# Kernel tuning notes

Hardware: AMD Instinct MI355X
Metric: run time of the kernel (lower is better)

The kernel has to match this reference:

```python
import jax, jax.numpy as jnp
import numpy as np

DIM, K, G, PAD = 384, 3, 4, 1
KK = K * K
EPS = 1e-5


def _deform_conv(x, offset, weight):
    # x: [B,C,H,W]; offset: [B,G*2*KK,H,W] (per group: (dy,dx) per tap); weight: [Cout,Cin,K,K]
    B, C, H, W = x.shape
    Cg = C // G
    off = offset.reshape(B, G, KK, 2, H, W)
    dy, dx = off[:, :, :, 0], off[:, :, :, 1]            # [B,G,KK,H,W]
    ky = (jnp.arange(KK) // K - PAD).astype(x.dtype).reshape(1, 1, KK, 1, 1)
    kx = (jnp.arange(KK) % K - PAD).astype(x.dtype).reshape(1, 1, KK, 1, 1)
    py = dy + ky + jnp.arange(H, dtype=x.dtype).reshape(1, 1, 1, H, 1)
    px = dx + kx + jnp.arange(W, dtype=x.dtype).reshape(1, 1, 1, 1, W)

    y0 = jnp.floor(py); x0 = jnp.floor(px)
    iy0 = y0.astype(jnp.int32); ix0 = x0.astype(jnp.int32)
    wy1 = py - y0; wx1 = px - x0
    img = x.reshape(B, G, Cg, H * W)[:, :, :, None, :]   # [B,G,Cg,1,HW]

    def corner(iy, ix, w):
        valid = (iy >= 0) & (iy < H) & (ix >= 0) & (ix < W)
        idx = (jnp.clip(iy, 0, H - 1) * W + jnp.clip(ix, 0, W - 1)).reshape(B, G, 1, KK, H * W)
        vals = jnp.take_along_axis(img, idx, axis=-1)    # [B,G,Cg,KK,HW]
        wm = (w * valid.astype(x.dtype)).reshape(B, G, 1, KK, H * W)
        return vals * wm

    sampled = (corner(iy0, ix0, (1 - wy1) * (1 - wx1))
               + corner(iy0, ix0 + 1, (1 - wy1) * wx1)
               + corner(iy0 + 1, ix0, wy1 * (1 - wx1))
               + corner(iy0 + 1, ix0 + 1, wy1 * wx1))    # [B,G,Cg,KK,HW]
    sampled = sampled.reshape(B, C, KK, H * W)
    out = jnp.einsum('bckp,ock->bop', sampled, weight.reshape(C, C, KK))
    return out.reshape(B, C, H, W)


def setup_inputs() -> dict:
    key = jax.random.key(0)
    ks = jax.random.split(key, 8)
    B, H, W = 8, 32, 32
    off_ch = G * 2 * KK
    return {
        'x': jax.random.normal(ks[0], (B, H * W, DIM), jnp.float32),
        'w_off': jax.random.normal(ks[1], (off_ch, DIM, 3, 3), jnp.float32) * 0.01,
        'b_off': jnp.zeros((off_ch,), jnp.float32),
        'w_dcn': jax.random.normal(ks[2], (DIM, DIM, K, K), jnp.float32) * 0.02,
        'bn_gamma': jnp.ones((DIM,), jnp.float32) + 0.1 * jax.random.normal(ks[3], (DIM,), jnp.float32),
        'bn_beta': 0.1 * jax.random.normal(ks[4], (DIM,), jnp.float32),
        'bn_mean': 0.1 * jax.random.normal(ks[5], (DIM,), jnp.float32),
        'bn_var': jax.random.uniform(ks[6], (DIM,), jnp.float32, 0.5, 1.5),
        'w2': jax.random.normal(ks[7], (DIM, DIM), jnp.float32) * 0.05,
        'b2': jnp.zeros((DIM,), jnp.float32),
        'H': H, 'W': W,
    }


def reference(x, w_off, b_off, w_dcn, bn_gamma, bn_beta, bn_mean, bn_var, w2, b2, H, W):
    B, P, C = x.shape
    xi = x.transpose(0, 2, 1).reshape(B, C, H, W)                       # [B,C,H,W]
    offset = jax.lax.conv_general_dilated(xi, w_off, (1, 1), ((1, 1), (1, 1)),
                                          dimension_numbers=('NCHW', 'OIHW', 'NCHW'))
    offset = offset + b_off[None, :, None, None]
    y = _deform_conv(xi, offset, w_dcn)
    # eval-mode BatchNorm2d + SiLU
    scale = bn_gamma / jnp.sqrt(bn_var + EPS)
    y = y * scale[None, :, None, None] + (bn_beta - bn_mean * scale)[None, :, None, None]
    y = y * jax.nn.sigmoid(y)
    # 1x1 conv
    y = jnp.einsum('bchw,oc->bohw', y, w2) + b2[None, :, None, None]
    return y.reshape(B, C, H * W).transpose(0, 2, 1)
```

## Files before the change

kernel.cpp:

```cpp
#include <hip/hip_runtime.h>
#include <math.h>

typedef _Float16 f16;
typedef _Float16 f16x2 __attribute__((ext_vector_type(2)));
typedef _Float16 f16x4 __attribute__((ext_vector_type(4)));
typedef _Float16 f16x8 __attribute__((ext_vector_type(8)));
typedef float f32x4 __attribute__((ext_vector_type(4)));

#define EPS_ 1e-5f

#define N_XP   3551232
#define N_WDCN 1327104
#define N_WOFF 331776
#define N_W2   147456
#define N_OFFS 589824
#define N_YH   3145728
#define N_AS   28311552

#define WS_NEED ((size_t)(N_XP + N_WDCN + N_WOFF + N_W2 + N_AS + N_YH) * 2 + (size_t)N_OFFS * 4)

static __device__ __forceinline__ f16x8 sp8(f16 h) { return (f16x8){h,h,h,h,h,h,h,h}; }

#define GLD_LDS16(g, l) __builtin_amdgcn_global_load_lds( \
    (const __attribute__((address_space(1))) void*)(g),   \
    (__attribute__((address_space(3))) void*)(l), 16, 0, 0)

#define VMCNT(N) asm volatile("s_waitcnt vmcnt(" #N ")" ::: "memory")

#define PK_X   786432
#define PK_XP  101376
#define PK_WD  147456
#define PK_WO  27648
#define PK_WZ  10368
#define PK_W2  147456
__global__ void k_pack(const float* __restrict__ x, const float* __restrict__ w_off,
                       const float* __restrict__ w_dcn, const float* __restrict__ w2,
                       f16* __restrict__ xp, f16* __restrict__ woffp,
                       f16* __restrict__ wdcnp, f16* __restrict__ w2p) {
    long i = (long)blockIdx.x * 256 + threadIdx.x;
    if (i < PK_X) {
        float4 v = ((const float4*)x)[i];
        f16x4 hv; hv.x = (f16)v.x; hv.y = (f16)v.y; hv.z = (f16)v.z; hv.w = (f16)v.w;
        int m = (int)(i / 96), c4 = (int)(i % 96);
        int b = m >> 10, h = (m >> 5) & 31, w = m & 31;
        long idx = ((long)(b * 34 + h + 1) * 34 + (w + 1)) * 96 + c4;
        ((f16x4*)xp)[idx] = hv;
    } else if (i < PK_X + PK_XP) {
        int j = (int)(i - PK_X);
        int cell = j / 96, c4 = j % 96;
        int b = cell / 132, p = cell % 132;
        int r, cp;
        if (p < 34)       { r = 0;          cp = p; }
        else if (p < 68)  { r = 33;         cp = p - 34; }
        else if (p < 100) { r = p - 68 + 1; cp = 0; }
        else              { r = p - 100 + 1; cp = 33; }
        long idx = ((long)(b * 34 + r) * 34 + cp) * 96 + c4;
        ((f16x4*)xp)[idx] = (f16x4){};
    } else if (i < PK_X + PK_XP + PK_WD) {
        int j = (int)(i - PK_X - PK_XP);
        int c = j % 384, oc = j / 384;
#pragma unroll
        for (int kk = 0; kk < 9; ++kk) {
            f16 v = (f16)w_dcn[(long)j * 9 + kk];
            wdcnp[(long)(kk * 6 + (c >> 6)) * 24576 + oc * 64 + (c & 63)] = v;
        }
    } else if (i < PK_X + PK_XP + PK_WD + PK_WO) {
        int j = (int)(i - PK_X - PK_XP - PK_WD);
        int c = j % 384, oc = j / 384;
#pragma unroll
        for (int kk = 0; kk < 9; ++kk) {
            f16 v = (f16)w_off[(long)j * 9 + kk];
            woffp[(long)(kk * 6 + (c >> 6)) * 6144 + oc * 64 + (c & 63)] = v;
        }
    } else if (i < PK_X + PK_XP + PK_WD + PK_WO + PK_WZ) {
        int j = (int)(i - PK_X - PK_XP - PK_WD - PK_WO);
        int ck = j / 192, r = j % 192;
        *(f16x8*)(&woffp[(long)ck * 6144 + 72 * 64 + r * 8]) = (f16x8){};
    } else if (i < PK_X + PK_XP + PK_WD + PK_WO + PK_WZ + PK_W2) {
        long j = i - (PK_X + PK_XP + PK_WD + PK_WO + PK_WZ);
        int kc = (int)(j & 63); long r = j >> 6;
        int oc = (int)(r % 384); int cc = (int)(r / 384);
        w2p[j] = (f16)w2[(long)oc * 384 + cc * 64 + kc];
    }
}

__global__ __launch_bounds__(256, 2) void k_off_gemm4(
        const f16* __restrict__ xp, const f16* __restrict__ wp,
        float* __restrict__ part) {
    __shared__ __attribute__((aligned(16))) f16 As[4][64 * 64];
    __shared__ __attribute__((aligned(16))) f16 Bs[4][96 * 64];
    int t = threadIdx.x;
    int bx = blockIdx.x;
    int ks = blockIdx.y;
    bx = (bx & 7) * 16 + (bx >> 3);
    int m0 = bx * 64;
    int w = t >> 6, l = t & 63, lr = l & 15, lq = l >> 4;
    int wmi = w & 1, wni = w >> 1;
    f32x4 acc[2][3] = {};

    const f16* a_base[2];
#pragma unroll
    for (int i = 0; i < 2; ++i) {
        int f = i * 256 + t;
        int ml = f >> 3, c8 = f & 7;
        int m = m0 + ml;
        int b = m >> 10, h = (m >> 5) & 31, ww = m & 31;
        a_base[i] = xp + ((long)(b * 34 + h + 1) * 34 + (ww + 1)) * 384 + ((c8 ^ (ml & 7)) * 8);
    }
    const f16* b_src[3];
#pragma unroll
    for (int i = 0; i < 3; ++i) {
        int f = i * 256 + t;
        int oc = f >> 3, c8 = f & 7;
        b_src[i] = wp + (long)oc * 64 + ((c8 ^ (oc & 7)) * 8);
    }

    int s_ck = (54 * ks) >> 2, e_ck = (54 * (ks + 1)) >> 2;
    int nck = e_ck - s_ck;

    auto stage = [&](int j, int buf) {
        int ck = s_ck + j;
        int kk = ck / 6, cc = ck % 6;
        int kkd = ((kk / 3 - 1) * 34 + (kk % 3 - 1)) * 384 + cc * 64;
#pragma unroll
        for (int i = 0; i < 2; ++i)
            GLD_LDS16(a_base[i] + kkd, &As[buf][i * 2048 + w * 512]);
#pragma unroll
        for (int i = 0; i < 3; ++i)
            GLD_LDS16(b_src[i] + (long)ck * 6144, &Bs[buf][i * 2048 + w * 512]);
    };
    auto compute = [&](int buf) {
        const char* Ab = (const char*)&As[buf][0];
        const char* Bb = (const char*)&Bs[buf][0];
        __builtin_amdgcn_s_setprio(1);
#pragma unroll
        for (int s = 0; s < 2; ++s) {
            int j = (s << 2) | lq;
            int swz = (j ^ (lr & 7)) * 16;
            f16x8 af[2], bf[3];
#pragma unroll
            for (int mi = 0; mi < 2; ++mi)
                af[mi] = *(const f16x8*)(Ab + (wmi * 32 + mi * 16 + lr) * 128 + swz);
#pragma unroll
            for (int n = 0; n < 3; ++n)
                bf[n] = *(const f16x8*)(Bb + (wni * 48 + n * 16 + lr) * 128 + swz);
#pragma unroll
            for (int mi = 0; mi < 2; ++mi)
#pragma unroll
                for (int n = 0; n < 3; ++n)
                    acc[mi][n] = __builtin_amdgcn_mfma_f32_16x16x32_f16(af[mi], bf[n], acc[mi][n], 0, 0, 0);
        }
        __builtin_amdgcn_s_setprio(0);
    };

    stage(0, 0);
    stage(1, 1);
    for (int j = 0; j < nck; ++j) {
        if (j + 2 < nck) {
            stage(j + 2, (j + 2) & 3);
            VMCNT(10);
        } else if (j + 1 < nck) {
            VMCNT(5);
        } else {
            VMCNT(0);
        }
        __builtin_amdgcn_s_barrier();
        compute(j & 3);
    }
    float* pb = part + (long)ks * (96 * 8192);
#pragma unroll
    for (int n = 0; n < 3; ++n) {
        int oc = wni * 48 + 16 * n + lr;
#pragma unroll
        for (int mi = 0; mi < 2; ++mi) {
            int m = m0 + wmi * 32 + 16 * mi + 4 * lq;
            *(f32x4*)(&pb[(long)oc * 8192 + m]) = acc[mi][n];
        }
    }
}

__global__ __launch_bounds__(256) void k_off_reduce(
        const float* __restrict__ part, const float* __restrict__ b_off,
        float* __restrict__ offs) {
    int j = blockIdx.x * 256 + threadIdx.x;
    int oc = j >> 11;
    int mq = (j & 2047) << 2;
    const long S = 96L * 8192;
    f32x4 s0 = *(const f32x4*)(&part[(long)oc * 8192 + mq]);
    f32x4 s1 = *(const f32x4*)(&part[S + (long)oc * 8192 + mq]);
    f32x4 s2 = *(const f32x4*)(&part[2 * S + (long)oc * 8192 + mq]);
    f32x4 s3 = *(const f32x4*)(&part[3 * S + (long)oc * 8192 + mq]);
    f32x4 s = s0 + s1 + s2 + s3;
    float b = b_off[oc];
#pragma unroll
    for (int r = 0; r < 4; ++r)
        offs[(long)(mq + r) * 72 + oc] = s[r] + b;
}

__global__ __launch_bounds__(256) void k_sample(
        const f16* __restrict__ xp, const float* __restrict__ offs,
        f16* __restrict__ A_t) {
    __shared__ int   cad[64][4][4];
    __shared__ f16x4 cwd[64][4];
    int t = threadIdx.x;
    int raw = blockIdx.x;
    int bx = (raw & 7) * 16 + (raw >> 3);
    int kk = blockIdx.y;
    int m0 = bx * 64;
    {
        int row = t & 63, g = t >> 6;
        int m = m0 + row;
        int b = m >> 10, h = (m >> 5) & 31, wpix = m & 31;
        const float2 o = *(const float2*)(offs + (long)m * 72 + (g * 9 + kk) * 2);
        float py = o.x + (float)(h + kk / 3 - 1);
        float px = o.y + (float)(wpix + kk % 3 - 1);
        float fy = floorf(py), fx = floorf(px);
        int iy0 = (int)fy, ix0 = (int)fx;
        float wy1 = py - fy, wx1 = px - fx;
        float wy0 = 1.f - wy1, wx0 = 1.f - wx1;
        bool vy0 = iy0 >= 0 && iy0 < 32, vy1 = iy0 + 1 >= 0 && iy0 + 1 < 32;
        bool vx0 = ix0 >= 0 && ix0 < 32, vx1 = ix0 + 1 >= 0 && ix0 + 1 < 32;
        int cy0 = min(max(iy0, 0), 31), cy1 = min(max(iy0 + 1, 0), 31);
        int cx0 = min(max(ix0, 0), 31), cx1 = min(max(ix0 + 1, 0), 31);
        cad[row][g][0] = ((b * 34 + cy0 + 1) * 34 + cx0 + 1) * 768;
        cad[row][g][1] = ((b * 34 + cy0 + 1) * 34 + cx1 + 1) * 768;
        cad[row][g][2] = ((b * 34 + cy1 + 1) * 34 + cx0 + 1) * 768;
        cad[row][g][3] = ((b * 34 + cy1 + 1) * 34 + cx1 + 1) * 768;
        f16x4 wv;
        wv.x = (f16)(wy0 * wx0 * ((vy0 && vx0) ? 1.f : 0.f));
        wv.y = (f16)(wy0 * wx1 * ((vy0 && vx1) ? 1.f : 0.f));
        wv.z = (f16)(wy1 * wx0 * ((vy1 && vx0) ? 1.f : 0.f));
        wv.w = (f16)(wy1 * wx1 * ((vy1 && vx1) ? 1.f : 0.f));
        cwd[row][g] = wv;
    }
    __syncthreads();
    int rb = t >> 3, w8 = t & 7;
    const char* xb = (const char*)xp;
    long obase = ((long)bx * 54 + (long)kk * 6) * 4096;
#pragma unroll
    for (int cc = 0; cc < 6; ++cc) {
        int c = cc * 64 + 8 * w8;
        int g = c / 96;
        long cb = (long)c * 2;
#pragma unroll
        for (int rr = 0; rr < 2; ++rr) {
            int r = 2 * rb + rr;
            const int* ca = cad[r][g];
            f16x4 wv = cwd[r][g];
            f16x8 v0 = *(const f16x8*)(xb + ca[0] + cb);
            f16x8 v1 = *(const f16x8*)(xb + ca[1] + cb);
            f16x8 v2 = *(const f16x8*)(xb + ca[2] + cb);
            f16x8 v3 = *(const f16x8*)(xb + ca[3] + cb);
            f16x8 ov = v0 * sp8(wv.x) + v1 * sp8(wv.y) + v2 * sp8(wv.z) + v3 * sp8(wv.w);
            *(f16x8*)(A_t + obase + cc * 4096 + r * 64 + ((w8 ^ (r & 7)) * 8)) = ov;
        }
    }
}

__global__ __launch_bounds__(256, 2) void k_dcn_gemm2(
        const f16* __restrict__ A_t, const f16* __restrict__ Bp,
        const float* __restrict__ bng, const float* __restrict__ bnb,
        const float* __restrict__ bnm, const float* __restrict__ bnv,
        f16* __restrict__ yh) {
    __shared__ __attribute__((aligned(16))) f16 As[4][64 * 64];
    __shared__ __attribute__((aligned(16))) f16 Bs[4][96 * 64];
    int t = threadIdx.x;
    int bx = blockIdx.x;
    bx = (bx & 7) * 16 + (bx >> 3);
    int m0 = bx * 64;
    int n0 = blockIdx.y * 96;
    int w = t >> 6, l = t & 63, lr = l & 15, lq = l >> 4;
    int wmi = w & 1, wni = w >> 1;
    f32x4 acc[2][3] = {};

    const f16* a_base = A_t + (long)bx * 54 * 4096 + t * 8;
    const f16* b_src[3];
#pragma unroll
    for (int i = 0; i < 3; ++i) {
        int f = i * 256 + t;
        int oc = f >> 3, c8 = f & 7;
        b_src[i] = Bp + (long)(n0 + oc) * 64 + ((c8 ^ (oc & 7)) * 8);
    }

    auto stage = [&](int ck, int buf) {
#pragma unroll
        for (int i = 0; i < 2; ++i)
            GLD_LDS16(a_base + (long)ck * 4096 + i * 2048, &As[buf][i * 2048 + w * 512]);
#pragma unroll
        for (int i = 0; i < 3; ++i)
            GLD_LDS16(b_src[i] + (long)ck * 24576, &Bs[buf][i * 2048 + w * 512]);
    };
    auto compute = [&](int buf) {
        const char* Ab = (const char*)&As[buf][0];
        const char* Bb = (const char*)&Bs[buf][0];
        __builtin_amdgcn_s_setprio(1);
#pragma unroll
        for (int s = 0; s < 2; ++s) {
            int j = (s << 2) | lq;
            int swz = (j ^ (lr & 7)) * 16;
            f16x8 af[2], bf[3];
#pragma unroll
            for (int mi = 0; mi < 2; ++mi)
                af[mi] = *(const f16x8*)(Ab + (wmi * 32 + mi * 16 + lr) * 128 + swz);
#pragma unroll
            for (int n = 0; n < 3; ++n)
                bf[n] = *(const f16x8*)(Bb + (wni * 48 + n * 16 + lr) * 128 + swz);
#pragma unroll
            for (int mi = 0; mi < 2; ++mi)
#pragma unroll
                for (int n = 0; n < 3; ++n)
                    acc[mi][n] = __builtin_amdgcn_mfma_f32_16x16x32_f16(af[mi], bf[n], acc[mi][n], 0, 0, 0);
        }
        __builtin_amdgcn_s_setprio(0);
    };

    stage(0, 0);
    stage(1, 1);
    for (int ck = 0; ck < 54; ++ck) {
        if (ck + 2 < 54) {
            stage(ck + 2, (ck + 2) & 3);
            VMCNT(10);
        } else if (ck + 1 < 54) {
            VMCNT(5);
        } else {
            VMCNT(0);
        }
        __builtin_amdgcn_s_barrier();
        compute(ck & 3);
    }
#pragma unroll
    for (int n = 0; n < 3; ++n) {
        int oc = n0 + wni * 48 + n * 16 + lr;
        float sc = bng[oc] * rsqrtf(bnv[oc] + EPS_);
        float shf = bnb[oc] - bnm[oc] * sc;
#pragma unroll
        for (int mi = 0; mi < 2; ++mi)
#pragma unroll
            for (int r = 0; r < 4; ++r) {
                int m = m0 + wmi * 32 + mi * 16 + 4 * lq + r;
                float v = acc[mi][n][r] * sc + shf;
                v = v / (1.f + __expf(-v));
                yh[(long)m * 384 + oc] = (f16)v;
            }
    }
}

__global__ __launch_bounds__(512, 2) void k_dcn_fused(
        const f16* __restrict__ xp, const float* __restrict__ offs,
        const f16* __restrict__ wp,
        const float* __restrict__ bng, const float* __restrict__ bnb,
        const float* __restrict__ bnm, const float* __restrict__ bnv,
        f16* __restrict__ yh) {
    __shared__ __attribute__((aligned(16))) f16 As[2][64 * 72];
    __shared__ __attribute__((aligned(16))) int ca[2][4][64][4];
    __shared__ __attribute__((aligned(16))) f16x4 cwl[2][4][64];
    int t = threadIdx.x;
    int bx = blockIdx.x;
    bx = (bx & 7) * 16 + (bx >> 3);
    int m0 = bx * 64;
    int n0 = blockIdx.y * 192;
    int w = t >> 6, l = t & 63, lr = l & 15, lq = l >> 4;
    int wm = (w & 1) * 32, wn = (w >> 1) * 48;
    int spx = t >> 3, slot = t & 7;
    const char* xb = (const char*)xp;
    f32x4 acc[2][3] = {};

    auto coords = [&](int kkn, int bufn) {
        if (t < 256) {
            int g = t >> 6, px = t & 63;
            int m = m0 + px;
            int b = m >> 10, h = (m >> 5) & 31, wwp = m & 31;
            int ky = kkn / 3 - 1, kx = kkn % 3 - 1;
            const float2 o = *(const float2*)(offs + (long)m * 72 + (g * 9 + kkn) * 2);
            float py = o.x + (float)(h + ky);
            float pxx = o.y + (float)(wwp + kx);
            float fy = floorf(py), fx = floorf(pxx);
            int iy0 = (int)fy, ix0 = (int)fx;
            float wy1 = py - fy, wx1 = pxx - fx;
            float wy0 = 1.f - wy1, wx0 = 1.f - wx1;
            bool vy0 = iy0 >= 0 && iy0 < 32, vy1 = iy0 + 1 >= 0 && iy0 + 1 < 32;
            bool vx0 = ix0 >= 0 && ix0 < 32, vx1 = ix0 + 1 >= 0 && ix0 + 1 < 32;
            int cy0 = min(max(iy0, 0), 31), cy1 = min(max(iy0 + 1, 0), 31);
            int cx0 = min(max(ix0, 0), 31), cx1 = min(max(ix0 + 1, 0), 31);
            ca[bufn][g][px][0] = ((b * 34 + cy0 + 1) * 34 + cx0 + 1) * 768;
            ca[bufn][g][px][1] = ((b * 34 + cy0 + 1) * 34 + cx1 + 1) * 768;
            ca[bufn][g][px][2] = ((b * 34 + cy1 + 1) * 34 + cx0 + 1) * 768;
            ca[bufn][g][px][3] = ((b * 34 + cy1 + 1) * 34 + cx1 + 1) * 768;
            f16x4 wv;
            wv.x = (f16)(wy0 * wx0 * ((vy0 && vx0) ? 1.f : 0.f));
            wv.y = (f16)(wy0 * wx1 * ((vy0 && vx1) ? 1.f : 0.f));
            wv.z = (f16)(wy1 * wx0 * ((vy1 && vx0) ? 1.f : 0.f));
            wv.w = (f16)(wy1 * wx1 * ((vy1 && vx1) ? 1.f : 0.f));
            cwl[bufn][g][px] = wv;
        }
    };

    coords(0, 0);
    __syncthreads();
    {
        int cst = 8 * slot;
        int g = cst / 96;
        int4 cv = *(const int4*)(&ca[0][g][spx][0]);
        f16x4 wv = cwl[0][g][spx];
        long cb = (long)(cst * 2);
        f16x8 v0 = *(const f16x8*)(xb + cv.x + cb);
        f16x8 v1 = *(const f16x8*)(xb + cv.y + cb);
        f16x8 v2 = *(const f16x8*)(xb + cv.z + cb);
        f16x8 v3 = *(const f16x8*)(xb + cv.w + cb);
        f16x8 sv = v0 * sp8(wv.x) + v1 * sp8(wv.y) + v2 * sp8(wv.z) + v3 * sp8(wv.w);
        *(f16x8*)(&As[0][spx * 72 + 8 * slot]) = sv;
    }
    int cur = 0, kk = 0, cc = 0;
    for (int ck = 0; ck < 54; ++ck) {
        __syncthreads();
        bool hn = ck < 53;
        int kk2 = kk + (cc == 5), cc2 = (cc == 5) ? 0 : (cc + 1);
        f16x8 v0, v1, v2, v3; f16x4 wv;
        if (hn) {
            int cst = cc2 * 64 + 8 * slot;
            int g = cst / 96;
            int kb = kk2 & 1;
            int4 cv = *(const int4*)(&ca[kb][g][spx][0]);
            wv = cwl[kb][g][spx];
            long cb = (long)(cst * 2);
            v0 = *(const f16x8*)(xb + cv.x + cb);
            v1 = *(const f16x8*)(xb + cv.y + cb);
            v2 = *(const f16x8*)(xb + cv.z + cb);
            v3 = *(const f16x8*)(xb + cv.w + cb);
        }
        if (cc == 4 && kk < 8) coords(kk + 1, (kk + 1) & 1);
        const f16* wbase = wp + (long)ck * (384 * 64);
#pragma unroll
        for (int s = 0; s < 2; ++s) {
            f16x8 a0 = *(const f16x8*)(&As[cur][(wm + lr) * 72 + 32 * s + 8 * lq]);
            f16x8 a1 = *(const f16x8*)(&As[cur][(wm + 16 + lr) * 72 + 32 * s + 8 * lq]);
#pragma unroll
            for (int n = 0; n < 3; ++n) {
                f16x8 b = *(const f16x8*)(wbase + (long)(n0 + wn + 16 * n + lr) * 64 + 32 * s + 8 * lq);
                acc[0][n] = __builtin_amdgcn_mfma_f32_16x16x32_f16(a0, b, acc[0][n], 0, 0, 0);
                acc[1][n] = __builtin_amdgcn_mfma_f32_16x16x32_f16(a1, b, acc[1][n], 0, 0, 0);
            }
        }
        if (hn) {
            f16x8 sv = v0 * sp8(wv.x) + v1 * sp8(wv.y) + v2 * sp8(wv.z) + v3 * sp8(wv.w);
            *(f16x8*)(&As[cur ^ 1][spx * 72 + 8 * slot]) = sv;
        }
        cur ^= 1; kk = kk2; cc = cc2;
    }
#pragma unroll
    for (int n = 0; n < 3; ++n) {
        int oc = n0 + wn + 16 * n + lr;
        float sc = bng[oc] * rsqrtf(bnv[oc] + EPS_);
        float sh = bnb[oc] - bnm[oc] * sc;
#pragma unroll
        for (int mi = 0; mi < 2; ++mi)
#pragma unroll
            for (int r = 0; r < 4; ++r) {
                int m = m0 + wm + 16 * mi + 4 * lq + r;
                float v = acc[mi][n][r] * sc + sh;
                v = v / (1.f + __expf(-v));
                yh[(long)m * 384 + oc] = (f16)v;
            }
    }
}

__global__ __launch_bounds__(256, 2) void k_out_gemm3(
        const f16* __restrict__ yh, const f16* __restrict__ wp,
        const float* __restrict__ b2, float* __restrict__ out) {
    __shared__ __attribute__((aligned(16))) f16 As[4][64 * 64];
    __shared__ __attribute__((aligned(16))) f16 Bs[4][96 * 64];
    int t = threadIdx.x;
    int bx = blockIdx.x;
    bx = (bx & 7) * 16 + (bx >> 3);
    int m0 = bx * 64;
    int n0 = blockIdx.y * 96;
    int w = t >> 6, l = t & 63, lr = l & 15, lq = l >> 4;
    int wmi = w & 1, wni = w >> 1;
    f32x4 acc[2][3] = {};

    const f16* a_src[2];
#pragma unroll
    for (int i = 0; i < 2; ++i) {
        int f = i * 256 + t;
        int ml = f >> 3, c8 = f & 7;
        a_src[i] = yh + (long)(m0 + ml) * 384 + ((c8 ^ (ml & 7)) * 8);
    }
    const f16* b_src[3];
#pragma unroll
    for (int i = 0; i < 3; ++i) {
        int f = i * 256 + t;
        int oc = f >> 3, c8 = f & 7;
        b_src[i] = wp + (long)(n0 + oc) * 64 + ((c8 ^ (oc & 7)) * 8);
    }

    auto stage = [&](int cc, int buf) {
#pragma unroll
        for (int i = 0; i < 2; ++i)
            GLD_LDS16(a_src[i] + cc * 64, &As[buf][i * 2048 + w * 512]);
#pragma unroll
        for (int i = 0; i < 3; ++i)
            GLD_LDS16(b_src[i] + (long)cc * 24576, &Bs[buf][i * 2048 + w * 512]);
    };
    auto compute = [&](int buf) {
        const char* Ab = (const char*)&As[buf][0];
        const char* Bb = (const char*)&Bs[buf][0];
        __builtin_amdgcn_s_setprio(1);
#pragma unroll
        for (int s = 0; s < 2; ++s) {
            int j = (s << 2) | lq;
            int swz = (j ^ (lr & 7)) * 16;
            f16x8 af[2], bf[3];
#pragma unroll
            for (int mi = 0; mi < 2; ++mi)
                af[mi] = *(const f16x8*)(Ab + (wmi * 32 + mi * 16 + lr) * 128 + swz);
#pragma unroll
            for (int n = 0; n < 3; ++n)
                bf[n] = *(const f16x8*)(Bb + (wni * 48 + n * 16 + lr) * 128 + swz);
#pragma unroll
            for (int mi = 0; mi < 2; ++mi)
#pragma unroll
                for (int n = 0; n < 3; ++n)
                    acc[mi][n] = __builtin_amdgcn_mfma_f32_16x16x32_f16(af[mi], bf[n], acc[mi][n], 0, 0, 0);
        }
        __builtin_amdgcn_s_setprio(0);
    };

    stage(0, 0);
    stage(1, 1);
    for (int cc = 0; cc < 6; ++cc) {
        if (cc + 2 < 6) {
            stage(cc + 2, (cc + 2) & 3);
            VMCNT(10);
        } else if (cc + 1 < 6) {
            VMCNT(5);
        } else {
            VMCNT(0);
        }
        __builtin_amdgcn_s_barrier();
        compute(cc & 3);
    }
#pragma unroll
    for (int n = 0; n < 3; ++n) {
        int oc = n0 + wni * 48 + 16 * n + lr;
        float bia = b2[oc];
#pragma unroll
        for (int mi = 0; mi < 2; ++mi)
#pragma unroll
            for (int r = 0; r < 4; ++r) {
                int m = m0 + wmi * 32 + 16 * mi + 4 * lq + r;
                out[(long)m * 384 + oc] = acc[mi][n][r] + bia;
            }
    }
}

extern "C" void kernel_launch(void* const* d_in, const int* in_sizes, int n_in,
                              void* d_out, int out_size, void* d_ws, size_t ws_size,
                              hipStream_t stream) {
    const float* x        = (const float*)d_in[0];
    const float* w_off    = (const float*)d_in[1];
    const float* b_off    = (const float*)d_in[2];
    const float* w_dcn    = (const float*)d_in[3];
    const float* bn_gamma = (const float*)d_in[4];
    const float* bn_beta  = (const float*)d_in[5];
    const float* bn_mean  = (const float*)d_in[6];
    const float* bn_var   = (const float*)d_in[7];
    const float* w2       = (const float*)d_in[8];
    const float* b2       = (const float*)d_in[9];

    char* ws = (char*)d_ws;
    f16*   xp    = (f16*)ws;                                  ws += (size_t)N_XP * 2;
    f16*   wdcnp = (f16*)ws;                                  ws += (size_t)N_WDCN * 2;
    f16*   woffp = (f16*)ws;                                  ws += (size_t)N_WOFF * 2;
    f16*   w2p   = (f16*)ws;                                  ws += (size_t)N_W2 * 2;
    float* offs  = (float*)ws;                                ws += (size_t)N_OFFS * 4;
    f16*   yh    = (f16*)ws;                                  ws += (size_t)N_YH * 2;
    f16*   A_t   = (f16*)ws;
    bool big = ws_size >= WS_NEED;
    float* part = (float*)(big ? (void*)A_t : (void*)ws);

    k_pack<<<4770, 256, 0, stream>>>(x, w_off, w_dcn, w2, xp, woffp, wdcnp, w2p);
    k_off_gemm4<<<dim3(128, 4), 256, 0, stream>>>(xp, woffp, part);
    k_off_reduce<<<576, 256, 0, stream>>>(part, b_off, offs);

    if (big) {
        k_sample<<<dim3(128, 9), 256, 0, stream>>>(xp, offs, A_t);
        k_dcn_gemm2<<<dim3(128, 4), 256, 0, stream>>>(A_t, wdcnp,
                bn_gamma, bn_beta, bn_mean, bn_var, yh);
    } else {
        k_dcn_fused<<<dim3(128, 2), 512, 0, stream>>>(xp, offs, wdcnp,
                bn_gamma, bn_beta, bn_mean, bn_var, yh);
    }
    k_out_gemm3<<<dim3(128, 4), 256, 0, stream>>>(yh, w2p, b2, (float*)d_out);
}
```

Baseline: 84.09 us.

## Load GEMM B fragments directly into registers and drop B shared-memory staging

In the deformable-conv GEMM and the output 1x1 GEMM, the weight (B) operand is now read from global memory straight into MFMA fragment registers, double-buffered across two k-chunks. It is no longer staged through swizzled LDS buffers. Removing the Bs arrays cuts LDS per block, so launch bounds are raised to allow 3 blocks per CU. The cost is duplicated global/L2 traffic for B across waves, more vector registers, and a retuned vmcnt wait scheme that has to match the new load counts.

Result: slower. 136.6 us (+62.4%).

```diff
diff --git a/kernel.cpp b/kernel.cpp
--- a/kernel.cpp
+++ b/kernel.cpp
@@ -257,13 +257,12 @@
     }
 }
 
-__global__ __launch_bounds__(256, 2) void k_dcn_gemm2(
+__global__ __launch_bounds__(256, 3) void k_dcn_gemm2(
         const f16* __restrict__ A_t, const f16* __restrict__ Bp,
         const float* __restrict__ bng, const float* __restrict__ bnb,
         const float* __restrict__ bnm, const float* __restrict__ bnv,
         f16* __restrict__ yh) {
     __shared__ __attribute__((aligned(16))) f16 As[4][64 * 64];
-    __shared__ __attribute__((aligned(16))) f16 Bs[4][96 * 64];
     int t = threadIdx.x;
     int bx = blockIdx.x;
     bx = (bx & 7) * 16 + (bx >> 3);
@@ -274,59 +273,57 @@
     f32x4 acc[2][3] = {};
 
     const f16* a_base = A_t + (long)bx * 54 * 4096 + t * 8;
-    const f16* b_src[3];
-#pragma unroll
-    for (int i = 0; i < 3; ++i) {
-        int f = i * 256 + t;
-        int oc = f >> 3, c8 = f & 7;
-        b_src[i] = Bp + (long)(n0 + oc) * 64 + ((c8 ^ (oc & 7)) * 8);
-    }
-
-    auto stage = [&](int ck, int buf) {
+    const f16* b_frag = Bp + (long)(n0 + wni * 48 + lr) * 64 + 8 * lq;
+
+    auto stageA = [&](int ck, int buf) {
 #pragma unroll
         for (int i = 0; i < 2; ++i)
             GLD_LDS16(a_base + (long)ck * 4096 + i * 2048, &As[buf][i * 2048 + w * 512]);
-#pragma unroll
-        for (int i = 0; i < 3; ++i)
-            GLD_LDS16(b_src[i] + (long)ck * 24576, &Bs[buf][i * 2048 + w * 512]);
-    };
-    auto compute = [&](int buf) {
+    };
+    auto ldB = [&](f16x8 bf[3][2], int ck) {
+        const f16* wb = b_frag + (long)ck * 24576;
+#pragma unroll
+        for (int n = 0; n < 3; ++n)
+#pragma unroll
+            for (int s = 0; s < 2; ++s)
+                bf[n][s] = *(const f16x8*)(wb + n * 16 * 64 + 32 * s);
+    };
+    auto compute = [&](int buf, f16x8 bf[3][2]) {
         const char* Ab = (const char*)&As[buf][0];
-        const char* Bb = (const char*)&Bs[buf][0];
         __builtin_amdgcn_s_setprio(1);
 #pragma unroll
         for (int s = 0; s < 2; ++s) {
             int j = (s << 2) | lq;
             int swz = (j ^ (lr & 7)) * 16;
-            f16x8 af[2], bf[3];
+            f16x8 af[2];
 #pragma unroll
             for (int mi = 0; mi < 2; ++mi)
                 af[mi] = *(const f16x8*)(Ab + (wmi * 32 + mi * 16 + lr) * 128 + swz);
 #pragma unroll
-            for (int n = 0; n < 3; ++n)
-                bf[n] = *(const f16x8*)(Bb + (wni * 48 + n * 16 + lr) * 128 + swz);
-#pragma unroll
             for (int mi = 0; mi < 2; ++mi)
 #pragma unroll
                 for (int n = 0; n < 3; ++n)
-                    acc[mi][n] = __builtin_amdgcn_mfma_f32_16x16x32_f16(af[mi], bf[n], acc[mi][n], 0, 0, 0);
+                    acc[mi][n] = __builtin_amdgcn_mfma_f32_16x16x32_f16(af[mi], bf[n][s], acc[mi][n], 0, 0, 0);
         }
         __builtin_amdgcn_s_setprio(0);
     };
 
-    stage(0, 0);
-    stage(1, 1);
-    for (int ck = 0; ck < 54; ++ck) {
-        if (ck + 2 < 54) {
-            stage(ck + 2, (ck + 2) & 3);
-            VMCNT(10);
-        } else if (ck + 1 < 54) {
-            VMCNT(5);
-        } else {
-            VMCNT(0);
-        }
+    f16x8 b0[3][2], b1[3][2];
+    stageA(0, 0);
+    stageA(1, 1);
+    ldB(b0, 0);
+    for (int c2 = 0; c2 < 27; ++c2) {
+        int ck = 2 * c2;
+        if (ck + 2 < 54) stageA(ck + 2, (ck + 2) & 3);
+        ldB(b1, ck + 1);
+        VMCNT(8);
         __builtin_amdgcn_s_barrier();
-        compute(ck & 3);
+        compute(ck & 3, b0);
+        if (ck + 3 < 54) stageA(ck + 3, (ck + 3) & 3);
+        if (ck + 2 < 54) { ldB(b0, ck + 2); VMCNT(8); }
+        else             { VMCNT(0); }
+        __builtin_amdgcn_s_barrier();
+        compute((ck + 1) & 3, b1);
     }
 #pragma unroll
     for (int n = 0; n < 3; ++n) {
@@ -464,11 +461,10 @@
     }
 }
 
-__global__ __launch_bounds__(256, 2) void k_out_gemm3(
+__global__ __launch_bounds__(256, 3) void k_out_gemm3(
         const f16* __restrict__ yh, const f16* __restrict__ wp,
         const float* __restrict__ b2, float* __restrict__ out) {
     __shared__ __attribute__((aligned(16))) f16 As[4][64 * 64];
-    __shared__ __attribute__((aligned(16))) f16 Bs[4][96 * 64];
     int t = threadIdx.x;
     int bx = blockIdx.x;
     bx = (bx & 7) * 16 + (bx >> 3);
@@ -485,59 +481,57 @@
         int ml = f >> 3, c8 = f & 7;
         a_src[i] = yh + (long)(m0 + ml) * 384 + ((c8 ^ (ml & 7)) * 8);
     }
-    const f16* b_src[3];
-#pragma unroll
-    for (int i = 0; i < 3; ++i) {
-        int f = i * 256 + t;
-        int oc = f >> 3, c8 = f & 7;
-        b_src[i] = wp + (long)(n0 + oc) * 64 + ((c8 ^ (oc & 7)) * 8);
-    }
-
-    auto stage = [&](int cc, int buf) {
+    const f16* b_frag = wp + (long)(n0 + wni * 48 + lr) * 64 + 8 * lq;
+
+    auto stageA = [&](int cc, int buf) {
 #pragma unroll
         for (int i = 0; i < 2; ++i)
             GLD_LDS16(a_src[i] + cc * 64, &As[buf][i * 2048 + w * 512]);
-#pragma unroll
-        for (int i = 0; i < 3; ++i)
-            GLD_LDS16(b_src[i] + (long)cc * 24576, &Bs[buf][i * 2048 + w * 512]);
-    };
-    auto compute = [&](int buf) {
+    };
+    auto ldB = [&](f16x8 bf[3][2], int cc) {
+        const f16* wb = b_frag + (long)cc * 24576;
+#pragma unroll
+        for (int n = 0; n < 3; ++n)
+#pragma unroll
+            for (int s = 0; s < 2; ++s)
+                bf[n][s] = *(const f16x8*)(wb + n * 16 * 64 + 32 * s);
+    };
+    auto compute = [&](int buf, f16x8 bf[3][2]) {
         const char* Ab = (const char*)&As[buf][0];
-        const char* Bb = (const char*)&Bs[buf][0];
         __builtin_amdgcn_s_setprio(1);
 #pragma unroll
         for (int s = 0; s < 2; ++s) {
             int j = (s << 2) | lq;
             int swz = (j ^ (lr & 7)) * 16;
-            f16x8 af[2], bf[3];
+            f16x8 af[2];
 #pragma unroll
             for (int mi = 0; mi < 2; ++mi)
                 af[mi] = *(const f16x8*)(Ab + (wmi * 32 + mi * 16 + lr) * 128 + swz);
 #pragma unroll
-            for (int n = 0; n < 3; ++n)
-                bf[n] = *(const f16x8*)(Bb + (wni * 48 + n * 16 + lr) * 128 + swz);
-#pragma unroll
             for (int mi = 0; mi < 2; ++mi)
 #pragma unroll
                 for (int n = 0; n < 3; ++n)
-                    acc[mi][n] = __builtin_amdgcn_mfma_f32_16x16x32_f16(af[mi], bf[n], acc[mi][n], 0, 0, 0);
+                    acc[mi][n] = __builtin_amdgcn_mfma_f32_16x16x32_f16(af[mi], bf[n][s], acc[mi][n], 0, 0, 0);
         }
         __builtin_amdgcn_s_setprio(0);
     };
 
-    stage(0, 0);
-    stage(1, 1);
-    for (int cc = 0; cc < 6; ++cc) {
-        if (cc + 2 < 6) {
-            stage(cc + 2, (cc + 2) & 3);
-            VMCNT(10);
-        } else if (cc + 1 < 6) {
-            VMCNT(5);
-        } else {
-            VMCNT(0);
-        }
+    f16x8 b0[3][2], b1[3][2];
+    stageA(0, 0);
+    stageA(1, 1);
+    ldB(b0, 0);
+    for (int c2 = 0; c2 < 3; ++c2) {
+        int cc = 2 * c2;
+        if (cc + 2 < 6) stageA(cc + 2, (cc + 2) & 3);
+        ldB(b1, cc + 1);
+        VMCNT(8);
         __builtin_amdgcn_s_barrier();
-        compute(cc & 3);
+        compute(cc & 3, b0);
+        if (cc + 3 < 6) stageA(cc + 3, (cc + 3) & 3);
+        if (cc + 2 < 6) { ldB(b0, cc + 2); VMCNT(8); }
+        else            { VMCNT(0); }
+        __builtin_amdgcn_s_barrier();
+        compute((cc + 1) & 3, b1);
     }
 #pragma unroll
     for (int n = 0; n < 3; ++n) {
```
